# Performance work log

Hardware: AMD Instinct MI355X
Metric: run time of the kernel (lower is better)

## Reference

```python
import jax, jax.numpy as jnp
import numpy as np

LATENT_CH = 64  # feature_ch // 8


def conv1x1(x, w):
    # Conv2dLayer with kernel_size=1, bias=False, activation='linear':
    # weight_gain = 1/sqrt(in_channels * 1)
    gain = 1.0 / np.sqrt(w.shape[1])
    return jnp.einsum('bchw,oc->bohw', x, w * gain)


def casual_attention(q, k, v):
    # q,k,v: [B, C, N] / [B, C, M]; score = q^T k, softmax over keys, out = score @ v^T
    score = jnp.einsum('bcn,bcm->bnm', q, k)
    score = jax.nn.softmax(score, axis=-1)
    return jnp.einsum('bnm,bcm->bnc', score, v)  # [B, N, C]


def reference(feature_map, concepts, w_theta, w_phi, w_g, w_o, gamma_sa, gamma_moca):
    B, C, H, W = feature_map.shape
    L = LATENT_CH
    HW = H * W

    # ---- SelfAttention ----
    th = conv1x1(feature_map, w_theta).reshape(B, L, HW)
    ph = conv1x1(feature_map, w_phi).reshape(B, L, HW)
    g = conv1x1(feature_map, w_g).reshape(B, L, HW)
    # torch does .view(-1, L, H, W) on a [B, HW, L] tensor -> raw memory reinterpret
    lat = casual_attention(th, ph, g).reshape(B, L, H, W)
    sa_out = gamma_sa * conv1x1(lat, w_o) + feature_map

    # ---- MomentumConceptAttention (theta and o shared with SA, trainable_conv=False) ----
    enc = conv1x1(sa_out, w_theta).reshape(B, L, HW)
    phi_c = concepts.T[None]                      # [1, L, P]  (torch.no_grad on concepts)
    phi_c = jnp.broadcast_to(phi_c, (B, L, concepts.shape[0]))
    lat2 = casual_attention(enc, phi_c, phi_c).reshape(B, L, H, W)
    out = gamma_moca * conv1x1(lat2, w_o) + sa_out
    return out


def setup_inputs() -> dict:
    key = jax.random.key(0)
    ks = jax.random.split(key, 8)
    B, C, H, W = 8, 512, 64, 64
    L, P = LATENT_CH, 256
    return {
        'feature_map': jax.random.normal(ks[0], (B, C, H, W), jnp.float32),
        'concepts': jax.random.normal(ks[1], (P, L), jnp.float32),
        'w_theta': jax.random.normal(ks[2], (L, C), jnp.float32),
        'w_phi': jax.random.normal(ks[3], (L, C), jnp.float32),
        'w_g': jax.random.normal(ks[4], (L, C), jnp.float32),
        'w_o': jax.random.normal(ks[5], (C, L), jnp.float32),
        'gamma_sa': jnp.float32(0.1),
        'gamma_moca': jnp.float32(0.1),
    }
```

## Files before the change

### kernel.cpp

```cpp
#include <hip/hip_runtime.h>
#include <math.h>

#define HW   4096
#define CINP 512
#define LCH  64

typedef short bf8 __attribute__((ext_vector_type(8)));
typedef float f4  __attribute__((ext_vector_type(4)));

__device__ __forceinline__ unsigned short f2bf(float x) {
    union { float f; unsigned int u; } v; v.f = x;
    return (unsigned short)((v.u + 0x7fffu + ((v.u >> 16) & 1u)) >> 16);
}
__device__ __forceinline__ bf8 ldbf8(const unsigned short* p) {
    uint4 u = *(const uint4*)p;
    return __builtin_bit_cast(bf8, u);
}

__global__ __launch_bounds__(256) void precast(
    const float* __restrict__ wt, const float* __restrict__ wp,
    const float* __restrict__ wg, const float* __restrict__ wo,
    const float* __restrict__ conc,
    unsigned short* __restrict__ WB, unsigned short* __restrict__ WO,
    unsigned short* __restrict__ CK, unsigned short* __restrict__ CV)
{
    const float gain = 0.04419417382415922f;
    int id = blockIdx.x * 256 + threadIdx.x;
    if (id < 98304) {
        int o = id >> 9, k = id & 511;
        const float* w = (o < 64) ? wt : (o < 128) ? wp : wg;
        WB[id] = f2bf(w[(o & 63) * 512 + k] * gain);
    } else if (id < 131072) {
        int j = id - 98304;
        WO[j] = f2bf(wo[j]);
    } else if (id < 147456) {
        int j = id - 131072;
        CK[j] = f2bf(conc[j]);
    } else if (id < 163840) {
        int j = id - 147456;
        int l = j >> 8, m = j & 255;
        CV[j] = f2bf(conc[m * 64 + l]);
    }
}

__global__ __launch_bounds__(256) void cast_transpose(const float* __restrict__ x,
                                                      unsigned short* __restrict__ XT)
{
    __shared__ unsigned short Lb[64][72];
    const int t  = threadIdx.x;
    const int n0 = blockIdx.x * 64, c0 = blockIdx.y * 64, b = blockIdx.z;
    const float* xb = x + ((size_t)b * CINP + c0) * HW + n0;
    const int cc = t >> 4, n4 = (t & 15) * 4;
    #pragma unroll
    for (int i = 0; i < 4; i++) {
        int c = cc + i * 16;
        float4 v = *(const float4*)(xb + (size_t)c * HW + n4);
        Lb[n4 + 0][c] = f2bf(v.x);
        Lb[n4 + 1][c] = f2bf(v.y);
        Lb[n4 + 2][c] = f2bf(v.z);
        Lb[n4 + 3][c] = f2bf(v.w);
    }
    __syncthreads();
    const int n = t & 63, cb0 = t >> 6;
    unsigned short* orow = XT + ((size_t)b * HW + n0 + n) * CINP + c0;
    #pragma unroll
    for (int i = 0; i < 2; i++) {
        int cb = cb0 + i * 4;
        *(uint4*)(orow + cb * 8) = *(const uint4*)&Lb[n][cb * 8];
    }
}

__global__ __launch_bounds__(256) void lat_transpose(const unsigned short* __restrict__ A,
                                                     unsigned short* __restrict__ LT)
{
    __shared__ unsigned short Ls[64][72];
    const int t = threadIdx.x, s0 = blockIdx.x * 64, b = blockIdx.y;
    const unsigned short* ab = A + (size_t)b * LCH * HW;
    #pragma unroll
    for (int it = 0; it < 2; it++) {
        int c = (t >> 3) + it * 32, s8 = (t & 7) * 8;
        union { uint4 u; unsigned short s[8]; } v;
        v.u = *(const uint4*)(ab + (size_t)c * HW + s0 + s8);
        #pragma unroll
        for (int i = 0; i < 8; i++) Ls[s8 + i][c] = v.s[i];
    }
    __syncthreads();
    unsigned short* ob = LT + ((size_t)b * HW + s0) * LCH;
    #pragma unroll
    for (int it = 0; it < 2; it++) {
        int s = (t >> 3) + it * 32, c8 = (t & 7);
        *(uint4*)(ob + (size_t)s * LCH + c8 * 8) = *(const uint4*)&Ls[s][c8 * 8];
    }
}

template <int NRT>
__global__ __launch_bounds__(256) void qkv_gemm(unsigned short* XT,
                                                const unsigned short* __restrict__ WB,
                                                unsigned short* __restrict__ VL)
{
    const int t = threadIdx.x;
    const int wave = t >> 6, lane = t & 63, quad = lane >> 4, lidx = lane & 15;
    const int b = blockIdx.y;
    const int ncol = blockIdx.x * 64 + wave * 16 + lidx;
    unsigned short* xrow = XT + ((size_t)b * HW + ncol) * CINP;

    f4 acc[NRT];
    #pragma unroll
    for (int r = 0; r < NRT; r++) acc[r] = (f4){0.f, 0.f, 0.f, 0.f};

    for (int kk = 0; kk < 16; kk++) {
        const int k0 = kk * 32 + quad * 8;
        bf8 bq = ldbf8(xrow + k0);
        #pragma unroll
        for (int rt = 0; rt < NRT; rt++) {
            bf8 aw = ldbf8(WB + (size_t)(rt * 16 + lidx) * CINP + k0);
            acc[rt] = __builtin_amdgcn_mfma_f32_16x16x32_bf16(aw, bq, acc[rt], 0, 0, 0);
        }
    }

    #pragma unroll
    for (int rt = 0; rt < NRT; rt++) {
        if (rt < 8) {
            union { unsigned short s[4]; uint2 u; } pk;
            #pragma unroll
            for (int r = 0; r < 4; r++) pk.s[r] = f2bf(acc[rt][r]);
            int off = (rt < 4) ? (rt * 16 + quad * 4) : (64 + (rt - 4) * 16 + quad * 4);
            *(uint2*)(xrow + off) = pk.u;
        } else {
            #pragma unroll
            for (int r = 0; r < 4; r++) {
                int l = (rt - 8) * 16 + quad * 4 + r;
                VL[((size_t)b * LCH + l) * HW + ncol] = f2bf(acc[rt][r]);
            }
        }
    }
}

__global__ __launch_bounds__(64) void flash(
    const unsigned short* Qb, size_t qbat,
    const unsigned short* Kb, size_t krow, size_t kbat,
    const unsigned short* Vb, size_t vrow, size_t vbat,
    unsigned short* __restrict__ Aout, int nkeys)
{
    __shared__ __align__(16) unsigned short Ps[2][32][40];

    const int lane = threadIdx.x, quad = lane >> 4, lidx = lane & 15;
    const int b = blockIdx.y, q0 = blockIdx.x * 32;
    const unsigned short* qp = Qb + (size_t)b * qbat;
    const unsigned short* kp = Kb + (size_t)b * kbat;
    const unsigned short* vp = Vb + (size_t)b * vbat;

    bf8 qa[2][2];
    #pragma unroll
    for (int qb = 0; qb < 2; qb++)
        #pragma unroll
        for (int kh = 0; kh < 2; kh++)
            qa[qb][kh] = ldbf8(qp + (size_t)(q0 + qb * 16 + lidx) * CINP + kh * 32 + quad * 8);

    f4 O[2][4];
    float Lp[2][4];
    #pragma unroll
    for (int qb = 0; qb < 2; qb++) {
        #pragma unroll
        for (int lt = 0; lt < 4; lt++) O[qb][lt] = (f4){0.f, 0.f, 0.f, 0.f};
        #pragma unroll
        for (int r = 0; r < 4; r++) Lp[qb][r] = 0.f;
    }

    const int ntiles = nkeys >> 5;
    #pragma unroll 2
    for (int tl = 0; tl < ntiles; tl++) {
        const int m0 = tl * 32;
        const unsigned short* kr0 = kp + (size_t)(m0 + lidx) * krow + quad * 8;
        const unsigned short* kr1 = kp + (size_t)(m0 + 16 + lidx) * krow + quad * 8;
        bf8 kf00 = ldbf8(kr0), kf01 = ldbf8(kr0 + 32);
        bf8 kf10 = ldbf8(kr1), kf11 = ldbf8(kr1 + 32);

        f4 S[2][2];
        #pragma unroll
        for (int qb = 0; qb < 2; qb++) {
            S[qb][0] = (f4){0.f, 0.f, 0.f, 0.f};
            S[qb][1] = (f4){0.f, 0.f, 0.f, 0.f};
            S[qb][0] = __builtin_amdgcn_mfma_f32_16x16x32_bf16(qa[qb][0], kf00, S[qb][0], 0, 0, 0);
            S[qb][0] = __builtin_amdgcn_mfma_f32_16x16x32_bf16(qa[qb][1], kf01, S[qb][0], 0, 0, 0);
            S[qb][1] = __builtin_amdgcn_mfma_f32_16x16x32_bf16(qa[qb][0], kf10, S[qb][1], 0, 0, 0);
            S[qb][1] = __builtin_amdgcn_mfma_f32_16x16x32_bf16(qa[qb][1], kf11, S[qb][1], 0, 0, 0);
        }

        const int pb = tl & 1;
        #pragma unroll
        for (int qb = 0; qb < 2; qb++)
            #pragma unroll
            for (int ms = 0; ms < 2; ms++)
                #pragma unroll
                for (int r = 0; r < 4; r++) {
                    float p = __expf(S[qb][ms][r]);
                    Lp[qb][r] += p;
                    Ps[pb][qb * 16 + quad * 4 + r][ms * 16 + lidx] = f2bf(p);
                }

        bf8 pf0 = *(const bf8*)&Ps[pb][lidx][quad * 8];
        bf8 pf1 = *(const bf8*)&Ps[pb][16 + lidx][quad * 8];

        #pragma unroll
        for (int lt = 0; lt < 4; lt++) {
            bf8 vf = ldbf8(vp + (size_t)(lt * 16 + lidx) * vrow + m0 + quad * 8);
            O[0][lt] = __builtin_amdgcn_mfma_f32_16x16x32_bf16(pf0, vf, O[0][lt], 0, 0, 0);
            O[1][lt] = __builtin_amdgcn_mfma_f32_16x16x32_bf16(pf1, vf, O[1][lt], 0, 0, 0);
        }
    }

    #pragma unroll
    for (int qb = 0; qb < 2; qb++) {
        float inv[4];
        #pragma unroll
        for (int r = 0; r < 4; r++) {
            float s = Lp[qb][r];
            s += __shfl_xor(s, 1);
            s += __shfl_xor(s, 2);
            s += __shfl_xor(s, 4);
            s += __shfl_xor(s, 8);
            inv[r] = 1.f / s;
        }
        #pragma unroll
        for (int lt = 0; lt < 4; lt++)
            #pragma unroll
            for (int r = 0; r < 4; r++) {
                size_t n = (size_t)b * HW + q0 + qb * 16 + quad * 4 + r;
                Aout[n * LCH + lt * 16 + lidx] = f2bf(O[qb][lt][r] * inv[r]);
            }
    }
}

__global__ __launch_bounds__(256) void conv_o(const unsigned short* __restrict__ LT,
                                              const unsigned short* __restrict__ WO,
                                              const float* __restrict__ res,
                                              const float* __restrict__ gamma_p,
                                              float* __restrict__ out,
                                              unsigned short* ST)
{
    const int t = threadIdx.x;
    const int wave = t >> 6, lane = t & 63, quad = lane >> 4, lidx = lane & 15;
    const int b = blockIdx.z, o0 = blockIdx.y * 64;
    const int scol = blockIdx.x * 64 + wave * 16 + lidx;
    const unsigned short* arow = LT + ((size_t)b * HW + scol) * LCH;

    f4 acc[4];
    #pragma unroll
    for (int ot = 0; ot < 4; ot++) acc[ot] = (f4){0.f, 0.f, 0.f, 0.f};

    #pragma unroll
    for (int kh = 0; kh < 2; kh++) {
        bf8 bq = ldbf8(arow + kh * 32 + quad * 8);
        #pragma unroll
        for (int ot = 0; ot < 4; ot++) {
            bf8 af = ldbf8(WO + (size_t)(o0 + ot * 16 + lidx) * LCH + kh * 32 + quad * 8);
            acc[ot] = __builtin_amdgcn_mfma_f32_16x16x32_bf16(af, bq, acc[ot], 0, 0, 0);
        }
    }

    const float scale = gamma_p[0] * 0.125f;
    #pragma unroll
    for (int ot = 0; ot < 4; ot++) {
        float v[4];
        #pragma unroll
        for (int r = 0; r < 4; r++) {
            size_t idx = ((size_t)b * CINP + o0 + ot * 16 + quad * 4 + r) * HW + scol;
            v[r] = fmaf(scale, acc[ot][r], res[idx]);
            out[idx] = v[r];
        }
        if (ST) {
            union { unsigned short s[4]; uint2 u; } pk;
            #pragma unroll
            for (int r = 0; r < 4; r++) pk.s[r] = f2bf(v[r]);
            *(uint2*)(ST + ((size_t)b * HW + scol) * CINP + o0 + ot * 16 + quad * 4) = pk.u;
        }
    }
}

extern "C" void kernel_launch(void* const* d_in, const int* in_sizes, int n_in,
                              void* d_out, int out_size, void* d_ws, size_t ws_size,
                              hipStream_t stream)
{
    const float* f    = (const float*)d_in[0];
    const float* conc = (const float*)d_in[1];
    const float* wt   = (const float*)d_in[2];
    const float* wp   = (const float*)d_in[3];
    const float* wg   = (const float*)d_in[4];
    const float* wo   = (const float*)d_in[5];
    const float* gsa  = (const float*)d_in[6];
    const float* gmo  = (const float*)d_in[7];
    float* out = (float*)d_out;

    char* ws = (char*)d_ws;
    unsigned short* XT = (unsigned short*)ws;
    unsigned short* VL = (unsigned short*)(ws + ((size_t)32 << 20));
    unsigned short* LT = VL;
    unsigned short* A1 = (unsigned short*)(ws + ((size_t)36 << 20));
    unsigned short* WB = (unsigned short*)(ws + ((size_t)40 << 20));
    unsigned short* WO = WB + 192 * 512;
    unsigned short* CK = WO + 512 * 64;
    unsigned short* CV = CK + 256 * 64;

    dim3 blk256(256), blk64(64);

    precast<<<640, blk256, 0, stream>>>(wt, wp, wg, wo, conc, WB, WO, CK, CV);
    cast_transpose<<<dim3(64, 8, 8), blk256, 0, stream>>>(f, XT);

    qkv_gemm<12><<<dim3(64, 8), blk256, 0, stream>>>(XT, WB, VL);
    flash<<<dim3(128, 8), blk64, 0, stream>>>(
        XT, (size_t)HW * CINP,
        XT + 64, CINP, (size_t)HW * CINP,
        VL, HW, (size_t)LCH * HW,
        A1, HW);
    lat_transpose<<<dim3(64, 8), blk256, 0, stream>>>(A1, LT);
    conv_o<<<dim3(64, 8, 8), blk256, 0, stream>>>(LT, WO, f, gsa, out, XT );

    qkv_gemm<4><<<dim3(64, 8), blk256, 0, stream>>>(XT , WB , nullptr);
    flash<<<dim3(128, 8), blk64, 0, stream>>>(
        XT, (size_t)HW * CINP,
        CK, LCH, 0,
        CV, 256, 0,
        A1 , 256);
    lat_transpose<<<dim3(64, 8), blk256, 0, stream>>>(A1, LT);
    conv_o<<<dim3(64, 8, 8), blk256, 0, stream>>>(LT, WO, out, gmo, out, nullptr);
}
```

Baseline: 417.8 us.

## Split flash attention keys across four waves per block with LDS reduction

The flash kernel now runs four waves per 32-query block, each handling a quarter of the key range. At the end, the waves combine their partial row sums and partial outputs through shared memory and write vectorized bf16 results. This raises parallelism from 1024 single-wave blocks to 1024 four-wave blocks, which should help hide latency in the long self-attention pass. The cost is extra LDS traffic and two block barriers. The softmax still uses no max subtraction, so the partial sums add directly.

```diff
diff --git a/kernel.cpp b/kernel.cpp
--- a/kernel.cpp
+++ b/kernel.cpp
@@ -136,19 +136,24 @@
     }
 }
 
-__global__ __launch_bounds__(64) void flash(
+__global__ __launch_bounds__(256) void flash(
     const unsigned short* Qb, size_t qbat,
     const unsigned short* Kb, size_t krow, size_t kbat,
     const unsigned short* Vb, size_t vrow, size_t vbat,
     unsigned short* __restrict__ Aout, int nkeys)
 {
-    __shared__ __align__(16) unsigned short Ps[2][32][40];
-
-    const int lane = threadIdx.x, quad = lane >> 4, lidx = lane & 15;
+    __shared__ __align__(16) char smem[4][8704];
+    __shared__ float Lw[4][32];
+
+    const int t = threadIdx.x;
+    const int wave = t >> 6, lane = t & 63, quad = lane >> 4, lidx = lane & 15;
     const int b = blockIdx.y, q0 = blockIdx.x * 32;
+    const int kw = nkeys >> 2;
+    const int kbase = wave * kw;
     const unsigned short* qp = Qb + (size_t)b * qbat;
     const unsigned short* kp = Kb + (size_t)b * kbat;
     const unsigned short* vp = Vb + (size_t)b * vbat;
+    unsigned short* psw = (unsigned short*)smem[wave];
 
     bf8 qa[2][2];
     #pragma unroll
@@ -167,10 +172,10 @@
         for (int r = 0; r < 4; r++) Lp[qb][r] = 0.f;
     }
 
-    const int ntiles = nkeys >> 5;
+    const int ntiles = kw >> 5;
     #pragma unroll 2
     for (int tl = 0; tl < ntiles; tl++) {
-        const int m0 = tl * 32;
+        const int m0 = kbase + tl * 32;
         const unsigned short* kr0 = kp + (size_t)(m0 + lidx) * krow + quad * 8;
         const unsigned short* kr1 = kp + (size_t)(m0 + 16 + lidx) * krow + quad * 8;
         bf8 kf00 = ldbf8(kr0), kf01 = ldbf8(kr0 + 32);
@@ -187,7 +192,7 @@
             S[qb][1] = __builtin_amdgcn_mfma_f32_16x16x32_bf16(qa[qb][1], kf11, S[qb][1], 0, 0, 0);
         }
 
-        const int pb = tl & 1;
+        const int pb = (tl & 1) * 32;
         #pragma unroll
         for (int qb = 0; qb < 2; qb++)
             #pragma unroll
@@ -196,11 +201,11 @@
                 for (int r = 0; r < 4; r++) {
                     float p = __expf(S[qb][ms][r]);
                     Lp[qb][r] += p;
-                    Ps[pb][qb * 16 + quad * 4 + r][ms * 16 + lidx] = f2bf(p);
+                    psw[(pb + qb * 16 + quad * 4 + r) * 40 + ms * 16 + lidx] = f2bf(p);
                 }
 
-        bf8 pf0 = *(const bf8*)&Ps[pb][lidx][quad * 8];
-        bf8 pf1 = *(const bf8*)&Ps[pb][16 + lidx][quad * 8];
+        bf8 pf0 = *(const bf8*)&psw[(pb + lidx) * 40 + quad * 8];
+        bf8 pf1 = *(const bf8*)&psw[(pb + 16 + lidx) * 40 + quad * 8];
 
         #pragma unroll
         for (int lt = 0; lt < 4; lt++) {
@@ -211,8 +216,7 @@
     }
 
     #pragma unroll
-    for (int qb = 0; qb < 2; qb++) {
-        float inv[4];
+    for (int qb = 0; qb < 2; qb++)
         #pragma unroll
         for (int r = 0; r < 4; r++) {
             float s = Lp[qb][r];
@@ -220,16 +224,39 @@
             s += __shfl_xor(s, 2);
             s += __shfl_xor(s, 4);
             s += __shfl_xor(s, 8);
-            inv[r] = 1.f / s;
-        }
+            if (lidx == 0) Lw[wave][qb * 16 + quad * 4 + r] = s;
+        }
+
+    __syncthreads();
+
+    float* opw = (float*)smem[wave];
+    #pragma unroll
+    for (int qb = 0; qb < 2; qb++)
         #pragma unroll
         for (int lt = 0; lt < 4; lt++)
             #pragma unroll
-            for (int r = 0; r < 4; r++) {
-                size_t n = (size_t)b * HW + q0 + qb * 16 + quad * 4 + r;
-                Aout[n * LCH + lt * 16 + lidx] = f2bf(O[qb][lt][r] * inv[r]);
-            }
-    }
+            for (int r = 0; r < 4; r++)
+                opw[(qb * 16 + quad * 4 + r) * 68 + lt * 16 + lidx] = O[qb][lt][r];
+
+    __syncthreads();
+
+    const int n = t >> 3, l0 = (t & 7) * 8;
+    const float inv = 1.f / (Lw[0][n] + Lw[1][n] + Lw[2][n] + Lw[3][n]);
+    float a0 = 0.f, a1 = 0.f, a2 = 0.f, a3 = 0.f, a4 = 0.f, a5 = 0.f, a6 = 0.f, a7 = 0.f;
+    #pragma unroll
+    for (int w = 0; w < 4; w++) {
+        const float* row = (const float*)smem[w] + n * 68 + l0;
+        float4 u = *(const float4*)row;
+        float4 v = *(const float4*)(row + 4);
+        a0 += u.x; a1 += u.y; a2 += u.z; a3 += u.w;
+        a4 += v.x; a5 += v.y; a6 += v.z; a7 += v.w;
+    }
+    union { unsigned short s[8]; uint4 u; } pk;
+    pk.s[0] = f2bf(a0 * inv); pk.s[1] = f2bf(a1 * inv);
+    pk.s[2] = f2bf(a2 * inv); pk.s[3] = f2bf(a3 * inv);
+    pk.s[4] = f2bf(a4 * inv); pk.s[5] = f2bf(a5 * inv);
+    pk.s[6] = f2bf(a6 * inv); pk.s[7] = f2bf(a7 * inv);
+    *(uint4*)(Aout + ((size_t)b * HW + q0 + n) * LCH + l0) = pk.u;
 }
 
 __global__ __launch_bounds__(256) void conv_o(const unsigned short* __restrict__ LT,
@@ -308,7 +335,7 @@
     cast_transpose<<<dim3(64, 8, 8), blk256, 0, stream>>>(f, XT);
 
     qkv_gemm<12><<<dim3(64, 8), blk256, 0, stream>>>(XT, WB, VL);
-    flash<<<dim3(128, 8), blk64, 0, stream>>>(
+    flash<<<dim3(128, 8), blk256, 0, stream>>>(
         XT, (size_t)HW * CINP,
         XT + 64, CINP, (size_t)HW * CINP,
         VL, HW, (size_t)LCH * HW,
@@ -317,7 +344,7 @@
     conv_o<<<dim3(64, 8, 8), blk256, 0, stream>>>(LT, WO, f, gsa, out, XT );
 
     qkv_gemm<4><<<dim3(64, 8), blk256, 0, stream>>>(XT , WB , nullptr);
-    flash<<<dim3(128, 8), blk64, 0, stream>>>(
+    flash<<<dim3(128, 8), blk256, 0, stream>>>(
         XT, (size_t)HW * CINP,
         CK, LCH, 0,
         CV, 256, 0,
```

Result: no change. 425.0 us (+1.7%).
